# Kernel tuning notes

Hardware: AMD Instinct MI355X
Metric: run time of the kernel (lower is better)

The kernel has to match this reference:

```python
import jax, jax.numpy as jnp
import numpy as np

M, B, U, D = 65536, 128, 256, 512
USAGE_DECAY = 0.95

def _l2n(x, axis):
    # tf.nn.l2_normalize semantics (K.l2_normalize)
    return x / jnp.sqrt(jnp.maximum(jnp.sum(x * x, axis=axis, keepdims=True), 1e-12))

def _lstm_cell(x, h, c, kernel, rec_kernel, bias):
    # Keras LSTMCell: gates in order i, f, c, o
    z = x @ kernel + h @ rec_kernel + bias  # [B, 4U]
    zi, zf, zc, zo = jnp.split(z, 4, axis=-1)
    i = jax.nn.sigmoid(zi)
    f = jax.nn.sigmoid(zf)
    c_new = f * c + i * jnp.tanh(zc)
    o = jax.nn.sigmoid(zo)
    h_new = o * jnp.tanh(c_new)
    return h_new, c_new

def setup_inputs() -> dict:
    key = jax.random.key(0)
    ks = jax.random.split(key, 10)
    return {
        "inputs": jax.random.normal(ks[0], (B, D), jnp.float32),
        "r_tm1": jnp.zeros((B, U), jnp.float32),
        "m_tm1": jax.random.uniform(ks[1], (M, U), jnp.float32),
        "c_wu_tm1": jax.random.uniform(ks[2], (M, B), jnp.float32),
        "c_wlu_tm1": jnp.zeros((M, B), jnp.float32),
        "c_wr_tm1": jax.random.uniform(ks[3], (M, B), jnp.float32),
        "h_tm1": jax.random.normal(ks[4], (B, U), jnp.float32) * 0.1,
        "cc_tm1": jax.random.normal(ks[5], (B, U), jnp.float32) * 0.1,
        "kernel": jax.random.normal(ks[6], (D + U, 4 * U), jnp.float32) * 0.02,
        "rec_kernel": jax.random.normal(ks[7], (U, 4 * U), jnp.float32) * 0.02,
        "bias": jnp.zeros((4 * U,), jnp.float32),
        "write_gate": jax.random.normal(ks[8], (1,), jnp.float32),
    }

def reference(inputs, r_tm1, m_tm1, c_wu_tm1, c_wlu_tm1, c_wr_tm1,
              h_tm1, cc_tm1, kernel, rec_kernel, bias, write_gate):
    # Controller step on [inputs, r_tm1]
    ctrl_in = jnp.concatenate([inputs, r_tm1], axis=1)          # [B, D+U]
    key_list, cc = _lstm_cell(ctrl_in, h_tm1, cc_tm1, kernel, rec_kernel, bias)  # [B, U]

    wg = jax.nn.sigmoid(write_gate)                              # [1]
    # NOTE: faithful to source -- scalar (1 - wg) is ADDED elementwise, then c_wlu added
    c_ww = wg * c_wr_tm1 + (1.0 - wg) + c_wlu_tm1                # [M, B]

    # cosine-similarity addressing
    cos = _l2n(key_list, 1) @ _l2n(m_tm1, 1).T                   # [B, M]
    # K.softmax on the transposed matrix => softmax over the BATCH axis (faithful)
    c_wr = jax.nn.softmax(cos.T, axis=-1)                        # [M, B]
    read = c_wr.T @ m_tm1                                        # [B, U]

    c_wu = USAGE_DECAY * c_wu_tm1 + c_wr + c_ww                  # [M, B]

    # top_k(c_wu.T, M): v.T[-1,:] is the per-batch minimum over slots
    mins = jnp.min(c_wu, axis=0)                                 # [B]
    min_idx = jnp.argmin(c_wu, axis=0)                           # [B]
    b_star = jnp.argmin(mins)                                    # scalar
    i_star = min_idx[b_star]                                     # global least-used slot

    c_wlu = (c_wu <= mins[None, :]).astype(jnp.float32)          # [M, B]

    # zeroing_matrix = one_hot(i_star broadcast to B cols, on=0, off=1) [M,B];
    # dot(zeroing[M,B], ones[B,U]) -> rows = B except zeroed row (faithful B scaling)
    keep = 1.0 - jax.nn.one_hot(i_star, M, dtype=jnp.float32)    # [M]
    memory = (float(B) * keep)[:, None] * m_tm1                  # [M, U]
    memory = c_ww @ key_list + memory                            # [M, U]

    return (read, memory, c_wu, c_wlu, c_wr, key_list, cc)
```

## Files before the change

### kernel.cpp

```cpp
#include <hip/hip_runtime.h>
#include <hip/hip_bf16.h>
#include <math.h>

#define NM 65536
#define NB 128
#define NU 256
#define ND 512

constexpr size_t OUT_READ = 0;
constexpr size_t OUT_MEM  = 32768;
constexpr size_t OUT_CWU  = OUT_MEM + 16777216;
constexpr size_t OUT_CWLU = OUT_CWU + 8388608;
constexpr size_t OUT_CWR  = OUT_CWLU + 8388608;
constexpr size_t OUT_KEY  = OUT_CWR + 8388608;
constexpr size_t OUT_CC   = OUT_KEY + 32768;

constexpr size_t WS_KLNT   = 0;
constexpr size_t WS_MINENC = 131072;
constexpr size_t WS_MINS   = 132096;
constexpr size_t WS_ISTAR  = 132608;
constexpr size_t WS_PART   = 135168;

typedef __attribute__((ext_vector_type(8))) short short8v;
typedef __attribute__((ext_vector_type(4))) float floatx4;

__device__ __forceinline__ unsigned fenc(float x) {
    unsigned u = __float_as_uint(x);
    return (u & 0x80000000u) ? ~u : (u | 0x80000000u);
}
__device__ __forceinline__ float fdec(unsigned e) {
    unsigned u = (e & 0x80000000u) ? (e ^ 0x80000000u) : ~e;
    return __uint_as_float(u);
}
__device__ __forceinline__ float sigm(float x) { return 1.0f / (1.0f + expf(-x)); }
__device__ __forceinline__ unsigned short f2b(float f) {
    __hip_bfloat16 h = __float2bfloat16(f);
    return *reinterpret_cast<unsigned short*>(&h);
}

__global__ __launch_bounds__(256) void k_lstm(
    const float* __restrict__ xin_g, const float* __restrict__ r_tm1,
    const float* __restrict__ h_tm1, const float* __restrict__ cc_tm1,
    const float* __restrict__ Wk, const float* __restrict__ Wr,
    const float* __restrict__ bias, float* __restrict__ out,
    float* __restrict__ klnT, unsigned long long* __restrict__ minenc)
{
    const int b = blockIdx.x, t = threadIdx.x;
    __shared__ float xin[ND + NU];
    __shared__ float hh[NU];
    __shared__ float red[NU];
    for (int k = t; k < ND; k += 256) xin[k] = xin_g[b * ND + k];
    xin[ND + t] = r_tm1[b * NU + t];
    hh[t] = h_tm1[b * NU + t];
    out[OUT_READ + b * NU + t] = 0.f;
    if (b == 0 && t < NB) minenc[t] = ~0ULL;
    __syncthreads();

    float zi = bias[t], zf = bias[NU + t], zc = bias[2 * NU + t], zo = bias[3 * NU + t];
    #pragma unroll 4
    for (int k = 0; k < ND + NU; ++k) {
        const float x = xin[k];
        const float* w = Wk + (size_t)k * (4 * NU);
        zi += x * w[t]; zf += x * w[NU + t]; zc += x * w[2 * NU + t]; zo += x * w[3 * NU + t];
    }
    #pragma unroll 4
    for (int k = 0; k < NU; ++k) {
        const float x = hh[k];
        const float* w = Wr + (size_t)k * (4 * NU);
        zi += x * w[t]; zf += x * w[NU + t]; zc += x * w[2 * NU + t]; zo += x * w[3 * NU + t];
    }
    const float gi = sigm(zi), gf = sigm(zf), gc = tanhf(zc), go = sigm(zo);
    const float cold = cc_tm1[b * NU + t];
    const float cn = __fadd_rn(__fmul_rn(gf, cold), __fmul_rn(gi, gc));
    const float hn = __fmul_rn(go, tanhf(cn));
    out[OUT_KEY + b * NU + t] = hn;
    out[OUT_CC + b * NU + t] = cn;
    red[t] = hn * hn;
    __syncthreads();
    for (int s = 128; s > 0; s >>= 1) { if (t < s) red[t] += red[t + s]; __syncthreads(); }
    const float nrm = sqrtf(fmaxf(red[0], 1e-12f));
    klnT[t * NB + b] = hn / nrm;
}

__global__ __launch_bounds__(256, 2) void k_dot(
    const float* __restrict__ mT, const float* __restrict__ klnT,
    const float* __restrict__ cwr_t, const float* __restrict__ cwlu_t,
    const float* __restrict__ cwu_t, const float* __restrict__ wgp,
    float* __restrict__ out, unsigned long long* __restrict__ minenc)
{
    __shared__ float smem[16384];
    __shared__ float rn_s[128];
    const int t = threadIdx.x, w = t >> 6, l = t & 63;
    const int tx = t & 15, ty = t >> 4;
    const int b0a = tx * 4, b0b = 64 + tx * 4;
    const int s0 = ty * 8;
    const int sb = blockIdx.x * 128;

    #pragma unroll 4
    for (int i = 0; i < 32; ++i) {
        const int s = w * 32 + i;
        const float4 mv = *(const float4*)(mT + (size_t)(sb + s) * NU + l * 4);
        float ss = mv.x * mv.x + mv.y * mv.y + mv.z * mv.z + mv.w * mv.w;
        #pragma unroll
        for (int d = 1; d < 64; d <<= 1) ss += __shfl_xor(ss, d);
        if (l == 0) rn_s[s] = sqrtf(fmaxf(ss, 1e-12f));
    }

    const int sl = t & 127, ug = t >> 7;
    const int ku_ = t >> 4, kb = (t & 15) * 4;

    float acc[8][8];
    #pragma unroll
    for (int i = 0; i < 8; ++i)
        #pragma unroll
        for (int j = 0; j < 8; ++j) acc[i][j] = 0.f;

    float4 gm[2], gk[2];
    #pragma unroll
    for (int i = 0; i < 2; ++i) {
        gm[i] = *(const float4*)(mT + (size_t)(sb + sl) * NU + (ug + 2 * i) * 4);
        gk[i] = *(const float4*)(klnT + (size_t)ku_ * NB + kb + i * 64);
    }
    for (int c = 0; c < 16; ++c) {
        const int mo = (c & 1) * 2048;
        const int ko = 4096 + (c & 1) * 2048;
        #pragma unroll
        for (int i = 0; i < 2; ++i) {
            const int uo = (ug + 2 * i) * 4;
            smem[mo + (uo + 0) * 128 + sl] = gm[i].x;
            smem[mo + (uo + 1) * 128 + sl] = gm[i].y;
            smem[mo + (uo + 2) * 128 + sl] = gm[i].z;
            smem[mo + (uo + 3) * 128 + sl] = gm[i].w;
            *(float4*)&smem[ko + ku_ * 128 + kb + i * 64] = gk[i];
        }
        __syncthreads();
        if (c < 15) {
            const int uc = (c + 1) * 16;
            #pragma unroll
            for (int i = 0; i < 2; ++i) {
                gm[i] = *(const float4*)(mT + (size_t)(sb + sl) * NU + uc + (ug + 2 * i) * 4);
                gk[i] = *(const float4*)(klnT + (size_t)(uc + ku_) * NB + kb + i * 64);
            }
        }
        #pragma unroll 4
        for (int u = 0; u < 16; ++u) {
            const float4 sv0 = *(const float4*)&smem[mo + u * 128 + s0];
            const float4 sv1 = *(const float4*)&smem[mo + u * 128 + s0 + 4];
            const float4 kv0 = *(const float4*)&smem[ko + u * 128 + b0a];
            const float4 kv1 = *(const float4*)&smem[ko + u * 128 + b0b];
            const float sv[8] = {sv0.x, sv0.y, sv0.z, sv0.w, sv1.x, sv1.y, sv1.z, sv1.w};
            const float kv[8] = {kv0.x, kv0.y, kv0.z, kv0.w, kv1.x, kv1.y, kv1.z, kv1.w};
            #pragma unroll
            for (int i = 0; i < 8; ++i)
                #pragma unroll
                for (int j = 0; j < 8; ++j)
                    acc[i][j] += sv[i] * kv[j];
        }
        __syncthreads();
    }

    #pragma unroll
    for (int i = 0; i < 8; ++i) {
        *(float4*)&smem[(s0 + i) * 128 + b0a] = make_float4(acc[i][0], acc[i][1], acc[i][2], acc[i][3]);
        *(float4*)&smem[(s0 + i) * 128 + b0b] = make_float4(acc[i][4], acc[i][5], acc[i][6], acc[i][7]);
    }
    __syncthreads();

    const float wg = sigm(wgp[0]);
    const float omw = __fsub_rn(1.f, wg);
    unsigned long long lmin0 = ~0ULL, lmin1 = ~0ULL;
    #pragma unroll 2
    for (int i = 0; i < 32; ++i) {
        const int s = w * 32 + i;
        const int m = sb + s;
        const float2 dv = *(const float2*)&smem[s * 128 + 2 * l];
        const float rnv = rn_s[s];
        const float2 wrt = ((const float2*)(cwr_t + (size_t)m * NB))[l];
        const float2 wlu = ((const float2*)(cwlu_t + (size_t)m * NB))[l];
        const float2 wut = ((const float2*)(cwu_t + (size_t)m * NB))[l];
        const float c0 = dv.x / rnv, c1 = dv.y / rnv;
        float mx = fmaxf(c0, c1);
        #pragma unroll
        for (int d = 1; d < 64; d <<= 1) mx = fmaxf(mx, __shfl_xor(mx, d));
        const float e0 = expf(c0 - mx), e1 = expf(c1 - mx);
        float sm = e0 + e1;
        #pragma unroll
        for (int d = 1; d < 64; d <<= 1) sm += __shfl_xor(sm, d);
        const float w0 = e0 / sm, w1 = e1 / sm;
        const float cww0 = __fadd_rn(__fadd_rn(__fmul_rn(wg, wrt.x), omw), wlu.x);
        const float cww1 = __fadd_rn(__fadd_rn(__fmul_rn(wg, wrt.y), omw), wlu.y);
        const float cu0 = __fadd_rn(__fadd_rn(__fmul_rn(0.95f, wut.x), w0), cww0);
        const float cu1 = __fadd_rn(__fadd_rn(__fmul_rn(0.95f, wut.y), w1), cww1);
        ((float2*)(out + OUT_CWR))[(size_t)m * 64 + l] = make_float2(w0, w1);
        ((float2*)(out + OUT_CWU))[(size_t)m * 64 + l] = make_float2(cu0, cu1);
        const unsigned long long e0u = (((unsigned long long)fenc(cu0)) << 32) | (unsigned)m;
        const unsigned long long e1u = (((unsigned long long)fenc(cu1)) << 32) | (unsigned)m;
        lmin0 = (e0u < lmin0) ? e0u : lmin0;
        lmin1 = (e1u < lmin1) ? e1u : lmin1;
    }
    atomicMin(&minenc[2 * l], lmin0);
    atomicMin(&minenc[2 * l + 1], lmin1);
}

__global__ void k_argmin(const unsigned long long* __restrict__ minenc,
                         float* __restrict__ mins, unsigned* __restrict__ istar)
{
    __shared__ unsigned long long red[NB];
    const int t = threadIdx.x;
    const unsigned long long e = minenc[t];
    const unsigned enc32 = (unsigned)(e >> 32);
    mins[t] = fdec(enc32);
    red[t] = (((unsigned long long)enc32) << 32) | (unsigned)t;
    __syncthreads();
    for (int s = 64; s > 0; s >>= 1) {
        if (t < s) { const unsigned long long o = red[t + s]; if (o < red[t]) red[t] = o; }
        __syncthreads();
    }
    if (t == 0) {
        const unsigned bstar = (unsigned)(red[0] & 0xFFFFFFFFu);
        istar[0] = (unsigned)(minenc[bstar] & 0xFFFFFFFFu);
    }
}

__global__ __launch_bounds__(256, 2) void k_mem(
    const float* __restrict__ mT,
    const float* __restrict__ cwr_t, const float* __restrict__ cwlu_t,
    const float* __restrict__ wgp, const float* __restrict__ mins,
    const unsigned* __restrict__ istar_p, float* __restrict__ out)
{
    __shared__ alignas(16) unsigned short cwwb[128 * 136];
    __shared__ alignas(16) unsigned short keyT[128 * 136];
    const int t = threadIdx.x, w = t >> 6, l = t & 63;
    const int sb = blockIdx.x * 128;
    const float wg = sigm(wgp[0]);
    const float omw = __fsub_rn(1.f, wg);
    const int istar = (int)istar_p[0];

    {
        const int srow = t >> 5;
        const int bc = (t & 31) * 4;
        for (int it = 0; it < 16; ++it) {
            const int s = it * 8 + srow;
            const size_t row = (size_t)(sb + s) * NB + bc;
            const float4 wr = *(const float4*)(cwr_t + row);
            const float4 lu = *(const float4*)(cwlu_t + row);
            const float4 wu = *(const float4*)(out + OUT_CWU + row);
            float4 cw;
            cw.x = __fadd_rn(__fadd_rn(__fmul_rn(wg, wr.x), omw), lu.x);
            cw.y = __fadd_rn(__fadd_rn(__fmul_rn(wg, wr.y), omw), lu.y);
            cw.z = __fadd_rn(__fadd_rn(__fmul_rn(wg, wr.z), omw), lu.z);
            cw.w = __fadd_rn(__fadd_rn(__fmul_rn(wg, wr.w), omw), lu.w);
            ushort4 pk;
            pk.x = f2b(cw.x); pk.y = f2b(cw.y); pk.z = f2b(cw.z); pk.w = f2b(cw.w);
            *(ushort4*)&cwwb[s * 136 + bc] = pk;
            const float4 mb = *(const float4*)(mins + bc);
            float4 wl;
            wl.x = (wu.x <= mb.x) ? 1.f : 0.f;
            wl.y = (wu.y <= mb.y) ? 1.f : 0.f;
            wl.z = (wu.z <= mb.z) ? 1.f : 0.f;
            wl.w = (wu.w <= mb.w) ? 1.f : 0.f;
            *(float4*)(out + OUT_CWLU + row) = wl;
        }
    }

    const int rk = (l >> 4) * 8;
    const int rr = l & 15;

    for (int uh = 0; uh < 2; ++uh) {
        if (uh) __syncthreads();
        {
            const int br = t >> 5;
            const int ko = (t & 31) * 4;
            for (int it = 0; it < 16; ++it) {
                const int b = it * 8 + br;
                const float4 kv = *(const float4*)(out + OUT_KEY + (size_t)b * NU + uh * 128 + ko);
                keyT[(ko + 0) * 136 + b] = f2b(kv.x);
                keyT[(ko + 1) * 136 + b] = f2b(kv.y);
                keyT[(ko + 2) * 136 + b] = f2b(kv.z);
                keyT[(ko + 3) * 136 + b] = f2b(kv.w);
            }
        }
        __syncthreads();

        floatx4 acc0[8], acc1[8];
        #pragma unroll
        for (int ut = 0; ut < 8; ++ut) {
            acc0[ut] = (floatx4){0.f, 0.f, 0.f, 0.f};
            acc1[ut] = (floatx4){0.f, 0.f, 0.f, 0.f};
        }
        #pragma unroll
        for (int kc = 0; kc < 4; ++kc) {
            const short8v a0 = *(const short8v*)&cwwb[(w * 32 + rr) * 136 + kc * 32 + rk];
            const short8v a1 = *(const short8v*)&cwwb[(w * 32 + 16 + rr) * 136 + kc * 32 + rk];
            #pragma unroll
            for (int ut = 0; ut < 8; ++ut) {
                const short8v bf = *(const short8v*)&keyT[(ut * 16 + rr) * 136 + kc * 32 + rk];
                acc0[ut] = __builtin_amdgcn_mfma_f32_16x16x32_bf16(a0, bf, acc0[ut], 0, 0, 0);
                acc1[ut] = __builtin_amdgcn_mfma_f32_16x16x32_bf16(a1, bf, acc1[ut], 0, 0, 0);
            }
        }

        __syncthreads();
        float* scr = (float*)keyT + w * 2112;
        const int erow = l >> 2, ecb = (l & 3) * 4;
        #pragma unroll
        for (int bt = 0; bt < 2; ++bt) {
            #pragma unroll
            for (int ut = 0; ut < 8; ++ut)
                #pragma unroll
                for (int q = 0; q < 4; ++q)
                    scr[((l >> 4) * 4 + q) * 132 + ut * 16 + rr] =
                        (bt == 0) ? acc0[ut][q] : acc1[ut][q];
            const int gs = sb + w * 32 + bt * 16 + erow;
            const float kf = (gs == istar) ? 0.f : 128.f;
            #pragma unroll
            for (int j = 0; j < 8; ++j) {
                const float4 d = *(const float4*)&scr[erow * 132 + j * 16 + ecb];
                const float4 mv = *(const float4*)(mT + (size_t)gs * NU + uh * 128 + j * 16 + ecb);
                float4 o;
                o.x = d.x + kf * mv.x;
                o.y = d.y + kf * mv.y;
                o.z = d.z + kf * mv.z;
                o.w = d.w + kf * mv.w;
                *(float4*)(out + OUT_MEM + (size_t)gs * NU + uh * 128 + j * 16 + ecb) = o;
            }
        }
    }
}

template <int USE_PART>
__global__ __launch_bounds__(256) void k_read(
    const float* __restrict__ mT, float* __restrict__ out, float* __restrict__ part)
{
    __shared__ alignas(16) unsigned short cwrb[128 * 40];
    __shared__ alignas(16) unsigned short mb[128 * 40];
    const int t = threadIdx.x, w = t >> 6, l = t & 63;
    const int r = blockIdx.x, ri = r >> 1, uh = r & 1;
    const int rk = (l >> 4) * 8, rr = l & 15;
    const float* cwr = out + OUT_CWR;
    const int srow = t >> 3, sc = (t & 7) * 16;

    floatx4 acc[2][8];
    #pragma unroll
    for (int bt = 0; bt < 2; ++bt)
        #pragma unroll
        for (int ut = 0; ut < 8; ++ut) acc[bt][ut] = (floatx4){0.f, 0.f, 0.f, 0.f};

    for (int c = 0; c < 8; ++c) {
        const size_t m0 = (size_t)(ri * 256 + c * 32);
        #pragma unroll
        for (int q = 0; q < 4; ++q) {
            const float4 v = *(const float4*)(cwr + (m0 + srow) * NB + sc + q * 4);
            cwrb[(sc + q * 4 + 0) * 40 + srow] = f2b(v.x);
            cwrb[(sc + q * 4 + 1) * 40 + srow] = f2b(v.y);
            cwrb[(sc + q * 4 + 2) * 40 + srow] = f2b(v.z);
            cwrb[(sc + q * 4 + 3) * 40 + srow] = f2b(v.w);
            const float4 u = *(const float4*)(mT + (m0 + srow) * NU + uh * 128 + sc + q * 4);
            mb[(sc + q * 4 + 0) * 40 + srow] = f2b(u.x);
            mb[(sc + q * 4 + 1) * 40 + srow] = f2b(u.y);
            mb[(sc + q * 4 + 2) * 40 + srow] = f2b(u.z);
            mb[(sc + q * 4 + 3) * 40 + srow] = f2b(u.w);
        }
        __syncthreads();
        const short8v a0 = *(const short8v*)&cwrb[(w * 32 + rr) * 40 + rk];
        const short8v a1 = *(const short8v*)&cwrb[(w * 32 + 16 + rr) * 40 + rk];
        #pragma unroll
        for (int ut = 0; ut < 8; ++ut) {
            const short8v bf = *(const short8v*)&mb[(ut * 16 + rr) * 40 + rk];
            acc[0][ut] = __builtin_amdgcn_mfma_f32_16x16x32_bf16(a0, bf, acc[0][ut], 0, 0, 0);
            acc[1][ut] = __builtin_amdgcn_mfma_f32_16x16x32_bf16(a1, bf, acc[1][ut], 0, 0, 0);
        }
        __syncthreads();
    }

    if (USE_PART) {
        float* dst = part + (size_t)r * (128 * 128);
        #pragma unroll
        for (int bt = 0; bt < 2; ++bt)
            #pragma unroll
            for (int ut = 0; ut < 8; ++ut)
                #pragma unroll
                for (int q = 0; q < 4; ++q)
                    dst[(size_t)(w * 32 + bt * 16 + (l >> 4) * 4 + q) * 128 + ut * 16 + rr] = acc[bt][ut][q];
    } else {
        #pragma unroll
        for (int bt = 0; bt < 2; ++bt)
            #pragma unroll
            for (int ut = 0; ut < 8; ++ut)
                #pragma unroll
                for (int q = 0; q < 4; ++q)
                    atomicAdd(out + OUT_READ + (size_t)(w * 32 + bt * 16 + (l >> 4) * 4 + q) * NU
                                  + uh * 128 + ut * 16 + rr, acc[bt][ut][q]);
    }
}

__global__ __launch_bounds__(256) void k_redread(const float* __restrict__ part,
                                                 float* __restrict__ out)
{
    const int b = blockIdx.x, u = threadIdx.x;
    const int uh = u >> 7, ul = u & 127;
    float s = 0.f;
    #pragma unroll 4
    for (int ri = 0; ri < 256; ++ri)
        s += part[((size_t)(ri * 2 + uh) * 128 + b) * 128 + ul];
    out[OUT_READ + b * NU + u] = s;
}

extern "C" void kernel_launch(void* const* d_in, const int* in_sizes, int n_in,
                              void* d_out, int out_size, void* d_ws, size_t ws_size,
                              hipStream_t stream)
{
    const float* inputs    = (const float*)d_in[0];
    const float* r_tm1     = (const float*)d_in[1];
    const float* m_tm1     = (const float*)d_in[2];
    const float* c_wu_tm1  = (const float*)d_in[3];
    const float* c_wlu_tm1 = (const float*)d_in[4];
    const float* c_wr_tm1  = (const float*)d_in[5];
    const float* h_tm1     = (const float*)d_in[6];
    const float* cc_tm1    = (const float*)d_in[7];
    const float* Wk        = (const float*)d_in[8];
    const float* Wr        = (const float*)d_in[9];
    const float* bias      = (const float*)d_in[10];
    const float* wgate     = (const float*)d_in[11];
    float* out = (float*)d_out;
    char* ws = (char*)d_ws;

    float* klnT = (float*)(ws + WS_KLNT);
    unsigned long long* minenc = (unsigned long long*)(ws + WS_MINENC);
    float* mins = (float*)(ws + WS_MINS);
    unsigned* istar = (unsigned*)(ws + WS_ISTAR);
    float* part = (float*)(ws + WS_PART);
    const bool use_part = ws_size >= WS_PART + (size_t)512 * 128 * 128 * 4;

    hipLaunchKernelGGL(k_lstm, dim3(128), dim3(256), 0, stream,
                       inputs, r_tm1, h_tm1, cc_tm1, Wk, Wr, bias, out, klnT, minenc);
    hipLaunchKernelGGL(k_dot, dim3(512), dim3(256), 0, stream,
                       m_tm1, klnT, c_wr_tm1, c_wlu_tm1, c_wu_tm1, wgate, out, minenc);
    hipLaunchKernelGGL(k_argmin, dim3(1), dim3(128), 0, stream, minenc, mins, istar);
    hipLaunchKernelGGL(k_mem, dim3(512), dim3(256), 0, stream,
                       m_tm1, c_wr_tm1, c_wlu_tm1, wgate, mins, istar, out);
    if (use_part) {
        hipLaunchKernelGGL((k_read<1>), dim3(512), dim3(256), 0, stream, m_tm1, out, part);
        hipLaunchKernelGGL(k_redread, dim3(128), dim3(256), 0, stream, part, out);
    } else {
        hipLaunchKernelGGL((k_read<0>), dim3(512), dim3(256), 0, stream, m_tm1, out, part);
    }
}
```

Before: 400.9 us.

## Split LSTM into wider gate kernel, fold argmin into merged mem/read kernel

The LSTM step is split into a 512-block gate kernel with 64 threads per block plus a separate norm kernel. The goal is more parallelism for the weight-streaming matvec, which previously ran on only 128 blocks. The single-block argmin kernel is removed, and each memory-update block now redoes the 128-entry argmin reduction itself. The memory-update and read kernels become one 1024-block launch, so the two independent workloads can run concurrently and launch gaps shrink. In exchange there is redundant argmin work per block, a larger LDS footprint, and one extra small launch for the norm.

New measurement: 418.8 us. 4.5% more time.

```diff
diff --git a/kernel.cpp b/kernel.cpp
--- a/kernel.cpp
+++ b/kernel.cpp
@@ -17,8 +17,6 @@
 
 constexpr size_t WS_KLNT   = 0;
 constexpr size_t WS_MINENC = 131072;
-constexpr size_t WS_MINS   = 132096;
-constexpr size_t WS_ISTAR  = 132608;
 constexpr size_t WS_PART   = 135168;
 
 typedef __attribute__((ext_vector_type(8))) short short8v;
@@ -38,43 +36,49 @@
     return *reinterpret_cast<unsigned short*>(&h);
 }
 
-__global__ __launch_bounds__(256) void k_lstm(
+__global__ __launch_bounds__(64) void k_gates(
     const float* __restrict__ xin_g, const float* __restrict__ r_tm1,
     const float* __restrict__ h_tm1, const float* __restrict__ cc_tm1,
     const float* __restrict__ Wk, const float* __restrict__ Wr,
     const float* __restrict__ bias, float* __restrict__ out,
-    float* __restrict__ klnT, unsigned long long* __restrict__ minenc)
-{
-    const int b = blockIdx.x, t = threadIdx.x;
+    unsigned long long* __restrict__ minenc)
+{
+    const int blk = blockIdx.x, t = threadIdx.x;
+    const int b = blk >> 2, u = (blk & 3) * 64 + t;
     __shared__ float xin[ND + NU];
     __shared__ float hh[NU];
-    __shared__ float red[NU];
-    for (int k = t; k < ND; k += 256) xin[k] = xin_g[b * ND + k];
-    xin[ND + t] = r_tm1[b * NU + t];
-    hh[t] = h_tm1[b * NU + t];
-    out[OUT_READ + b * NU + t] = 0.f;
-    if (b == 0 && t < NB) minenc[t] = ~0ULL;
+    for (int k = t; k < ND; k += 64) xin[k] = xin_g[b * ND + k];
+    for (int k = t; k < NU; k += 64) { xin[ND + k] = r_tm1[b * NU + k]; hh[k] = h_tm1[b * NU + k]; }
+    if (blk == 0) { minenc[t] = ~0ULL; minenc[t + 64] = ~0ULL; }
     __syncthreads();
 
-    float zi = bias[t], zf = bias[NU + t], zc = bias[2 * NU + t], zo = bias[3 * NU + t];
+    float zi = bias[u], zf = bias[NU + u], zc = bias[2 * NU + u], zo = bias[3 * NU + u];
     #pragma unroll 4
     for (int k = 0; k < ND + NU; ++k) {
         const float x = xin[k];
-        const float* w = Wk + (size_t)k * (4 * NU);
-        zi += x * w[t]; zf += x * w[NU + t]; zc += x * w[2 * NU + t]; zo += x * w[3 * NU + t];
+        const float* wp = Wk + (size_t)k * (4 * NU);
+        zi += x * wp[u]; zf += x * wp[NU + u]; zc += x * wp[2 * NU + u]; zo += x * wp[3 * NU + u];
     }
     #pragma unroll 4
     for (int k = 0; k < NU; ++k) {
         const float x = hh[k];
-        const float* w = Wr + (size_t)k * (4 * NU);
-        zi += x * w[t]; zf += x * w[NU + t]; zc += x * w[2 * NU + t]; zo += x * w[3 * NU + t];
+        const float* wp = Wr + (size_t)k * (4 * NU);
+        zi += x * wp[u]; zf += x * wp[NU + u]; zc += x * wp[2 * NU + u]; zo += x * wp[3 * NU + u];
     }
     const float gi = sigm(zi), gf = sigm(zf), gc = tanhf(zc), go = sigm(zo);
-    const float cold = cc_tm1[b * NU + t];
+    const float cold = cc_tm1[b * NU + u];
     const float cn = __fadd_rn(__fmul_rn(gf, cold), __fmul_rn(gi, gc));
     const float hn = __fmul_rn(go, tanhf(cn));
-    out[OUT_KEY + b * NU + t] = hn;
-    out[OUT_CC + b * NU + t] = cn;
+    out[OUT_KEY + b * NU + u] = hn;
+    out[OUT_CC + b * NU + u] = cn;
+}
+
+__global__ __launch_bounds__(256) void k_norm(float* __restrict__ out, float* __restrict__ klnT)
+{
+    const int b = blockIdx.x, t = threadIdx.x;
+    __shared__ float red[NU];
+    const float hn = out[OUT_KEY + b * NU + t];
+    out[OUT_READ + b * NU + t] = 0.f;
     red[t] = hn * hn;
     __syncthreads();
     for (int s = 128; s > 0; s >>= 1) { if (t < s) red[t] += red[t + s]; __syncthreads(); }
@@ -202,195 +206,187 @@
     atomicMin(&minenc[2 * l + 1], lmin1);
 }
 
-__global__ void k_argmin(const unsigned long long* __restrict__ minenc,
-                         float* __restrict__ mins, unsigned* __restrict__ istar)
-{
-    __shared__ unsigned long long red[NB];
-    const int t = threadIdx.x;
-    const unsigned long long e = minenc[t];
-    const unsigned enc32 = (unsigned)(e >> 32);
-    mins[t] = fdec(enc32);
-    red[t] = (((unsigned long long)enc32) << 32) | (unsigned)t;
-    __syncthreads();
-    for (int s = 64; s > 0; s >>= 1) {
-        if (t < s) { const unsigned long long o = red[t + s]; if (o < red[t]) red[t] = o; }
-        __syncthreads();
-    }
-    if (t == 0) {
-        const unsigned bstar = (unsigned)(red[0] & 0xFFFFFFFFu);
-        istar[0] = (unsigned)(minenc[bstar] & 0xFFFFFFFFu);
-    }
-}
-
-__global__ __launch_bounds__(256, 2) void k_mem(
+template <int USE_PART>
+__global__ __launch_bounds__(256) void k_memread(
     const float* __restrict__ mT,
     const float* __restrict__ cwr_t, const float* __restrict__ cwlu_t,
-    const float* __restrict__ wgp, const float* __restrict__ mins,
-    const unsigned* __restrict__ istar_p, float* __restrict__ out)
-{
-    __shared__ alignas(16) unsigned short cwwb[128 * 136];
-    __shared__ alignas(16) unsigned short keyT[128 * 136];
+    const float* __restrict__ wgp,
+    const unsigned long long* __restrict__ minenc,
+    float* __restrict__ out, float* __restrict__ part)
+{
+    __shared__ alignas(16) char ldsb[69632];
+    __shared__ float minsb_s[128];
+    __shared__ unsigned long long redm[128];
     const int t = threadIdx.x, w = t >> 6, l = t & 63;
-    const int sb = blockIdx.x * 128;
-    const float wg = sigm(wgp[0]);
-    const float omw = __fsub_rn(1.f, wg);
-    const int istar = (int)istar_p[0];
-
-    {
-        const int srow = t >> 5;
-        const int bc = (t & 31) * 4;
-        for (int it = 0; it < 16; ++it) {
-            const int s = it * 8 + srow;
-            const size_t row = (size_t)(sb + s) * NB + bc;
-            const float4 wr = *(const float4*)(cwr_t + row);
-            const float4 lu = *(const float4*)(cwlu_t + row);
-            const float4 wu = *(const float4*)(out + OUT_CWU + row);
-            float4 cw;
-            cw.x = __fadd_rn(__fadd_rn(__fmul_rn(wg, wr.x), omw), lu.x);
-            cw.y = __fadd_rn(__fadd_rn(__fmul_rn(wg, wr.y), omw), lu.y);
-            cw.z = __fadd_rn(__fadd_rn(__fmul_rn(wg, wr.z), omw), lu.z);
-            cw.w = __fadd_rn(__fadd_rn(__fmul_rn(wg, wr.w), omw), lu.w);
-            ushort4 pk;
-            pk.x = f2b(cw.x); pk.y = f2b(cw.y); pk.z = f2b(cw.z); pk.w = f2b(cw.w);
-            *(ushort4*)&cwwb[s * 136 + bc] = pk;
-            const float4 mb = *(const float4*)(mins + bc);
-            float4 wl;
-            wl.x = (wu.x <= mb.x) ? 1.f : 0.f;
-            wl.y = (wu.y <= mb.y) ? 1.f : 0.f;
-            wl.z = (wu.z <= mb.z) ? 1.f : 0.f;
-            wl.w = (wu.w <= mb.w) ? 1.f : 0.f;
-            *(float4*)(out + OUT_CWLU + row) = wl;
-        }
-    }
-
-    const int rk = (l >> 4) * 8;
-    const int rr = l & 15;
-
-    for (int uh = 0; uh < 2; ++uh) {
-        if (uh) __syncthreads();
+    const int rk = (l >> 4) * 8, rr = l & 15;
+
+    if (blockIdx.x < 512) {
+        unsigned short* cwwb = (unsigned short*)ldsb;
+        unsigned short* keyT = (unsigned short*)(ldsb + 34816);
+        const int sb = blockIdx.x * 128;
+        const float wg = sigm(wgp[0]);
+        const float omw = __fsub_rn(1.f, wg);
+
+        if (t < 128) {
+            const unsigned long long e = minenc[t];
+            const unsigned enc32 = (unsigned)(e >> 32);
+            minsb_s[t] = fdec(enc32);
+            redm[t] = (((unsigned long long)enc32) << 32) | (unsigned)t;
+        }
+        __syncthreads();
+        for (int s = 64; s > 0; s >>= 1) {
+            if (t < s) { const unsigned long long o = redm[t + s]; if (o < redm[t]) redm[t] = o; }
+            __syncthreads();
+        }
+        const unsigned bstar = (unsigned)(redm[0] & 0xFFFFFFFFu);
+        const int istar = (int)(unsigned)(minenc[bstar] & 0xFFFFFFFFu);
+
         {
-            const int br = t >> 5;
-            const int ko = (t & 31) * 4;
+            const int srow = t >> 5;
+            const int bc = (t & 31) * 4;
             for (int it = 0; it < 16; ++it) {
-                const int b = it * 8 + br;
-                const float4 kv = *(const float4*)(out + OUT_KEY + (size_t)b * NU + uh * 128 + ko);
-                keyT[(ko + 0) * 136 + b] = f2b(kv.x);
-                keyT[(ko + 1) * 136 + b] = f2b(kv.y);
-                keyT[(ko + 2) * 136 + b] = f2b(kv.z);
-                keyT[(ko + 3) * 136 + b] = f2b(kv.w);
-            }
-        }
-        __syncthreads();
-
-        floatx4 acc0[8], acc1[8];
-        #pragma unroll
-        for (int ut = 0; ut < 8; ++ut) {
-            acc0[ut] = (floatx4){0.f, 0.f, 0.f, 0.f};
-            acc1[ut] = (floatx4){0.f, 0.f, 0.f, 0.f};
-        }
-        #pragma unroll
-        for (int kc = 0; kc < 4; ++kc) {
-            const short8v a0 = *(const short8v*)&cwwb[(w * 32 + rr) * 136 + kc * 32 + rk];
-            const short8v a1 = *(const short8v*)&cwwb[(w * 32 + 16 + rr) * 136 + kc * 32 + rk];
+                const int s = it * 8 + srow;
+                const size_t row = (size_t)(sb + s) * NB + bc;
+                const float4 wr = *(const float4*)(cwr_t + row);
+                const float4 lu = *(const float4*)(cwlu_t + row);
+                const float4 wu = *(const float4*)(out + OUT_CWU + row);
+                float4 cw;
+                cw.x = __fadd_rn(__fadd_rn(__fmul_rn(wg, wr.x), omw), lu.x);
+                cw.y = __fadd_rn(__fadd_rn(__fmul_rn(wg, wr.y), omw), lu.y);
+                cw.z = __fadd_rn(__fadd_rn(__fmul_rn(wg, wr.z), omw), lu.z);
+                cw.w = __fadd_rn(__fadd_rn(__fmul_rn(wg, wr.w), omw), lu.w);
+                ushort4 pk;
+                pk.x = f2b(cw.x); pk.y = f2b(cw.y); pk.z = f2b(cw.z); pk.w = f2b(cw.w);
+                *(ushort4*)&cwwb[s * 136 + bc] = pk;
+                const float4 mb4 = *(const float4*)&minsb_s[bc];
+                float4 wl;
+                wl.x = (wu.x <= mb4.x) ? 1.f : 0.f;
+                wl.y = (wu.y <= mb4.y) ? 1.f : 0.f;
+                wl.z = (wu.z <= mb4.z) ? 1.f : 0.f;
+                wl.w = (wu.w <= mb4.w) ? 1.f : 0.f;
+                *(float4*)(out + OUT_CWLU + row) = wl;
+            }
+        }
+
+        for (int uh = 0; uh < 2; ++uh) {
+            if (uh) __syncthreads();
+            {
+                const int br = t >> 5;
+                const int ko = (t & 31) * 4;
+                for (int it = 0; it < 16; ++it) {
+                    const int b = it * 8 + br;
+                    const float4 kv = *(const float4*)(out + OUT_KEY + (size_t)b * NU + uh * 128 + ko);
+                    keyT[(ko + 0) * 136 + b] = f2b(kv.x);
+                    keyT[(ko + 1) * 136 + b] = f2b(kv.y);
+                    keyT[(ko + 2) * 136 + b] = f2b(kv.z);
+                    keyT[(ko + 3) * 136 + b] = f2b(kv.w);
+                }
+            }
+            __syncthreads();
+
+            floatx4 acc0[8], acc1[8];
             #pragma unroll
             for (int ut = 0; ut < 8; ++ut) {
-                const short8v bf = *(const short8v*)&keyT[(ut * 16 + rr) * 136 + kc * 32 + rk];
-                acc0[ut] = __builtin_amdgcn_mfma_f32_16x16x32_bf16(a0, bf, acc0[ut], 0, 0, 0);
-                acc1[ut] = __builtin_amdgcn_mfma_f32_16x16x32_bf16(a1, bf, acc1[ut], 0, 0, 0);
-            }
-        }
-
-        __syncthreads();
-        float* scr = (float*)keyT + w * 2112;
-        const int erow = l >> 2, ecb = (l & 3) * 4;
-        #pragma unroll
-        for (int bt = 0; bt < 2; ++bt) {
-            #pragma unroll
-            for (int ut = 0; ut < 8; ++ut)
-                #pragma unroll
-                for (int q = 0; q < 4; ++q)
-                    scr[((l >> 4) * 4 + q) * 132 + ut * 16 + rr] =
-                        (bt == 0) ? acc0[ut][q] : acc1[ut][q];
-            const int gs = sb + w * 32 + bt * 16 + erow;
-            const float kf = (gs == istar) ? 0.f : 128.f;
-            #pragma unroll
-            for (int j = 0; j < 8; ++j) {
-                const float4 d = *(const float4*)&scr[erow * 132 + j * 16 + ecb];
-                const float4 mv = *(const float4*)(mT + (size_t)gs * NU + uh * 128 + j * 16 + ecb);
-                float4 o;
-                o.x = d.x + kf * mv.x;
-                o.y = d.y + kf * mv.y;
-                o.z = d.z + kf * mv.z;
-                o.w = d.w + kf * mv.w;
-                *(float4*)(out + OUT_MEM + (size_t)gs * NU + uh * 128 + j * 16 + ecb) = o;
-            }
-        }
-    }
-}
-
-template <int USE_PART>
-__global__ __launch_bounds__(256) void k_read(
-    const float* __restrict__ mT, float* __restrict__ out, float* __restrict__ part)
-{
-    __shared__ alignas(16) unsigned short cwrb[128 * 40];
-    __shared__ alignas(16) unsigned short mb[128 * 40];
-    const int t = threadIdx.x, w = t >> 6, l = t & 63;
-    const int r = blockIdx.x, ri = r >> 1, uh = r & 1;
-    const int rk = (l >> 4) * 8, rr = l & 15;
-    const float* cwr = out + OUT_CWR;
-    const int srow = t >> 3, sc = (t & 7) * 16;
-
-    floatx4 acc[2][8];
-    #pragma unroll
-    for (int bt = 0; bt < 2; ++bt)
-        #pragma unroll
-        for (int ut = 0; ut < 8; ++ut) acc[bt][ut] = (floatx4){0.f, 0.f, 0.f, 0.f};
-
-    for (int c = 0; c < 8; ++c) {
-        const size_t m0 = (size_t)(ri * 256 + c * 32);
-        #pragma unroll
-        for (int q = 0; q < 4; ++q) {
-            const float4 v = *(const float4*)(cwr + (m0 + srow) * NB + sc + q * 4);
-            cwrb[(sc + q * 4 + 0) * 40 + srow] = f2b(v.x);
-            cwrb[(sc + q * 4 + 1) * 40 + srow] = f2b(v.y);
-            cwrb[(sc + q * 4 + 2) * 40 + srow] = f2b(v.z);
-            cwrb[(sc + q * 4 + 3) * 40 + srow] = f2b(v.w);
-            const float4 u = *(const float4*)(mT + (m0 + srow) * NU + uh * 128 + sc + q * 4);
-            mb[(sc + q * 4 + 0) * 40 + srow] = f2b(u.x);
-            mb[(sc + q * 4 + 1) * 40 + srow] = f2b(u.y);
-            mb[(sc + q * 4 + 2) * 40 + srow] = f2b(u.z);
-            mb[(sc + q * 4 + 3) * 40 + srow] = f2b(u.w);
-        }
-        __syncthreads();
-        const short8v a0 = *(const short8v*)&cwrb[(w * 32 + rr) * 40 + rk];
-        const short8v a1 = *(const short8v*)&cwrb[(w * 32 + 16 + rr) * 40 + rk];
-        #pragma unroll
-        for (int ut = 0; ut < 8; ++ut) {
-            const short8v bf = *(const short8v*)&mb[(ut * 16 + rr) * 40 + rk];
-            acc[0][ut] = __builtin_amdgcn_mfma_f32_16x16x32_bf16(a0, bf, acc[0][ut], 0, 0, 0);
-            acc[1][ut] = __builtin_amdgcn_mfma_f32_16x16x32_bf16(a1, bf, acc[1][ut], 0, 0, 0);
-        }
-        __syncthreads();
-    }
-
-    if (USE_PART) {
-        float* dst = part + (size_t)r * (128 * 128);
+                acc0[ut] = (floatx4){0.f, 0.f, 0.f, 0.f};
+                acc1[ut] = (floatx4){0.f, 0.f, 0.f, 0.f};
+            }
+            #pragma unroll
+            for (int kc = 0; kc < 4; ++kc) {
+                const short8v a0 = *(const short8v*)&cwwb[(w * 32 + rr) * 136 + kc * 32 + rk];
+                const short8v a1 = *(const short8v*)&cwwb[(w * 32 + 16 + rr) * 136 + kc * 32 + rk];
+                #pragma unroll
+                for (int ut = 0; ut < 8; ++ut) {
+                    const short8v bf = *(const short8v*)&keyT[(ut * 16 + rr) * 136 + kc * 32 + rk];
+                    acc0[ut] = __builtin_amdgcn_mfma_f32_16x16x32_bf16(a0, bf, acc0[ut], 0, 0, 0);
+                    acc1[ut] = __builtin_amdgcn_mfma_f32_16x16x32_bf16(a1, bf, acc1[ut], 0, 0, 0);
+                }
+            }
+
+            __syncthreads();
+            float* scr = (float*)keyT + w * 2112;
+            const int erow = l >> 2, ecb = (l & 3) * 4;
+            #pragma unroll
+            for (int bt = 0; bt < 2; ++bt) {
+                #pragma unroll
+                for (int ut = 0; ut < 8; ++ut)
+                    #pragma unroll
+                    for (int q = 0; q < 4; ++q)
+                        scr[((l >> 4) * 4 + q) * 132 + ut * 16 + rr] =
+                            (bt == 0) ? acc0[ut][q] : acc1[ut][q];
+                const int gs = sb + w * 32 + bt * 16 + erow;
+                const float kf = (gs == istar) ? 0.f : 128.f;
+                #pragma unroll
+                for (int j = 0; j < 8; ++j) {
+                    const float4 d = *(const float4*)&scr[erow * 132 + j * 16 + ecb];
+                    const float4 mv = *(const float4*)(mT + (size_t)gs * NU + uh * 128 + j * 16 + ecb);
+                    float4 o;
+                    o.x = d.x + kf * mv.x;
+                    o.y = d.y + kf * mv.y;
+                    o.z = d.z + kf * mv.z;
+                    o.w = d.w + kf * mv.w;
+                    *(float4*)(out + OUT_MEM + (size_t)gs * NU + uh * 128 + j * 16 + ecb) = o;
+                }
+            }
+        }
+    } else {
+        unsigned short* cwrb = (unsigned short*)ldsb;
+        unsigned short* mb   = (unsigned short*)(ldsb + 10240);
+        const int r = blockIdx.x - 512, ri = r >> 1, uh = r & 1;
+        const float* cwr = out + OUT_CWR;
+        const int srow = t >> 3, sc = (t & 7) * 16;
+
+        floatx4 acc[2][8];
         #pragma unroll
         for (int bt = 0; bt < 2; ++bt)
             #pragma unroll
-            for (int ut = 0; ut < 8; ++ut)
-                #pragma unroll
-                for (int q = 0; q < 4; ++q)
-                    dst[(size_t)(w * 32 + bt * 16 + (l >> 4) * 4 + q) * 128 + ut * 16 + rr] = acc[bt][ut][q];
-    } else {
-        #pragma unroll
-        for (int bt = 0; bt < 2; ++bt)
-            #pragma unroll
-            for (int ut = 0; ut < 8; ++ut)
-                #pragma unroll
-                for (int q = 0; q < 4; ++q)
-                    atomicAdd(out + OUT_READ + (size_t)(w * 32 + bt * 16 + (l >> 4) * 4 + q) * NU
-                                  + uh * 128 + ut * 16 + rr, acc[bt][ut][q]);
+            for (int ut = 0; ut < 8; ++ut) acc[bt][ut] = (floatx4){0.f, 0.f, 0.f, 0.f};
+
+        for (int c = 0; c < 8; ++c) {
+            const size_t m0 = (size_t)(ri * 256 + c * 32);
+            #pragma unroll
+            for (int q = 0; q < 4; ++q) {
+                const float4 v = *(const float4*)(cwr + (m0 + srow) * NB + sc + q * 4);
+                cwrb[(sc + q * 4 + 0) * 40 + srow] = f2b(v.x);
+                cwrb[(sc + q * 4 + 1) * 40 + srow] = f2b(v.y);
+                cwrb[(sc + q * 4 + 2) * 40 + srow] = f2b(v.z);
+                cwrb[(sc + q * 4 + 3) * 40 + srow] = f2b(v.w);
+                const float4 u = *(const float4*)(mT + (m0 + srow) * NU + uh * 128 + sc + q * 4);
+                mb[(sc + q * 4 + 0) * 40 + srow] = f2b(u.x);
+                mb[(sc + q * 4 + 1) * 40 + srow] = f2b(u.y);
+                mb[(sc + q * 4 + 2) * 40 + srow] = f2b(u.z);
+                mb[(sc + q * 4 + 3) * 40 + srow] = f2b(u.w);
+            }
+            __syncthreads();
+            const short8v a0 = *(const short8v*)&cwrb[(w * 32 + rr) * 40 + rk];
+            const short8v a1 = *(const short8v*)&cwrb[(w * 32 + 16 + rr) * 40 + rk];
+            #pragma unroll
+            for (int ut = 0; ut < 8; ++ut) {
+                const short8v bf = *(const short8v*)&mb[(ut * 16 + rr) * 40 + rk];
+                acc[0][ut] = __builtin_amdgcn_mfma_f32_16x16x32_bf16(a0, bf, acc[0][ut], 0, 0, 0);
+                acc[1][ut] = __builtin_amdgcn_mfma_f32_16x16x32_bf16(a1, bf, acc[1][ut], 0, 0, 0);
+            }
+            __syncthreads();
+        }
+
+        if (USE_PART) {
+            float* dst = part + (size_t)r * (128 * 128);
+            #pragma unroll
+            for (int bt = 0; bt < 2; ++bt)
+                #pragma unroll
+                for (int ut = 0; ut < 8; ++ut)
+                    #pragma unroll
+                    for (int q = 0; q < 4; ++q)
+                        dst[(size_t)(w * 32 + bt * 16 + (l >> 4) * 4 + q) * 128 + ut * 16 + rr] = acc[bt][ut][q];
+        } else {
+            #pragma unroll
+            for (int bt = 0; bt < 2; ++bt)
+                #pragma unroll
+                for (int ut = 0; ut < 8; ++ut)
+                    #pragma unroll
+                    for (int q = 0; q < 4; ++q)
+                        atomicAdd(out + OUT_READ + (size_t)(w * 32 + bt * 16 + (l >> 4) * 4 + q) * NU
+                                      + uh * 128 + ut * 16 + rr, acc[bt][ut][q]);
+        }
     }
 }
 
@@ -427,22 +423,20 @@
 
     float* klnT = (float*)(ws + WS_KLNT);
     unsigned long long* minenc = (unsigned long long*)(ws + WS_MINENC);
-    float* mins = (float*)(ws + WS_MINS);
-    unsigned* istar = (unsigned*)(ws + WS_ISTAR);
     float* part = (float*)(ws + WS_PART);
     const bool use_part = ws_size >= WS_PART + (size_t)512 * 128 * 128 * 4;
 
-    hipLaunchKernelGGL(k_lstm, dim3(128), dim3(256), 0, stream,
-                       inputs, r_tm1, h_tm1, cc_tm1, Wk, Wr, bias, out, klnT, minenc);
+    hipLaunchKernelGGL(k_gates, dim3(512), dim3(64), 0, stream,
+                       inputs, r_tm1, h_tm1, cc_tm1, Wk, Wr, bias, out, minenc);
+    hipLaunchKernelGGL(k_norm, dim3(128), dim3(256), 0, stream, out, klnT);
     hipLaunchKernelGGL(k_dot, dim3(512), dim3(256), 0, stream,
                        m_tm1, klnT, c_wr_tm1, c_wlu_tm1, c_wu_tm1, wgate, out, minenc);
-    hipLaunchKernelGGL(k_argmin, dim3(1), dim3(128), 0, stream, minenc, mins, istar);
-    hipLaunchKernelGGL(k_mem, dim3(512), dim3(256), 0, stream,
-                       m_tm1, c_wr_tm1, c_wlu_tm1, wgate, mins, istar, out);
     if (use_part) {
-        hipLaunchKernelGGL((k_read<1>), dim3(512), dim3(256), 0, stream, m_tm1, out, part);
+        hipLaunchKernelGGL((k_memread<1>), dim3(1024), dim3(256), 0, stream,
+                           m_tm1, c_wr_tm1, c_wlu_tm1, wgate, minenc, out, part);
         hipLaunchKernelGGL(k_redread, dim3(128), dim3(256), 0, stream, part, out);
     } else {
-        hipLaunchKernelGGL((k_read<0>), dim3(512), dim3(256), 0, stream, m_tm1, out, part);
-    }
-}
+        hipLaunchKernelGGL((k_memread<0>), dim3(1024), dim3(256), 0, stream,
+                           m_tm1, c_wr_tm1, c_wlu_tm1, wgate, minenc, out, part);
+    }
+}
```
